# Kernel tuning notes

Hardware: AMD Instinct MI355X
Metric: run time of the kernel (lower is better)

Reference implementation:

```python
import jax, jax.numpy as jnp
import numpy as np

T_HID, A_HID, V_HID = 256, 128, 128
LEN = T_HID + A_HID + V_HID            # 512
TIME_WINDOW = 2
EXT_DIM = TIME_WINDOW * LEN + 1        # 1025
RANK, OUT_DIM = 128, 16
STRIDE = 2
B, T = 256, 128
T_IN, A_IN, V_IN = 768, 74, 35


def _mk_lstm(key, d_in, h):
    k1, k2, k3 = jax.random.split(key, 3)
    s = 1.0 / np.sqrt(h)
    W_ih = jax.random.uniform(k1, (4 * h, d_in), jnp.float32, -s, s)
    W_hh = jax.random.uniform(k2, (4 * h, h), jnp.float32, -s, s)
    b = jax.random.uniform(k3, (4 * h,), jnp.float32, -s, s)
    return W_ih, W_hh, b


def setup_inputs() -> dict:
    key = jax.random.key(0)
    ks = jax.random.split(key, 10)
    inp = {
        "text_x": jax.random.normal(ks[0], (B, T, T_IN), jnp.float32),
        "audio_x": jax.random.normal(ks[1], (B, T, A_IN), jnp.float32),
        "video_x": jax.random.normal(ks[2], (B, T, V_IN), jnp.float32),
    }
    inp["W_ih_t"], inp["W_hh_t"], inp["b_t"] = _mk_lstm(ks[3], T_IN, T_HID)
    inp["W_ih_a"], inp["W_hh_a"], inp["b_a"] = _mk_lstm(ks[4], A_IN, A_HID)
    inp["W_ih_v"], inp["W_hh_v"], inp["b_v"] = _mk_lstm(ks[5], V_IN, V_HID)
    ro = RANK * OUT_DIM
    inp["W1"] = jax.random.normal(ks[6], (ro, LEN), jnp.float32) / np.sqrt(LEN)
    inp["b1"] = jnp.zeros((ro,), jnp.float32)
    inp["W2"] = jax.random.normal(ks[7], (ro, EXT_DIM), jnp.float32) / np.sqrt(EXT_DIM)
    inp["b2"] = jnp.zeros((ro,), jnp.float32)
    inp["fusion_w"] = jax.random.normal(ks[8], (1, RANK), jnp.float32) * np.sqrt(2.0 / (1 + RANK))
    return inp


def _lstm(x, W_ih, W_hh, b, h):
    # x: [B,T,D] -> all hidden states [B,T,H]; PyTorch gate order i,f,g,o
    xp = jnp.einsum('btd,gd->btg', x, W_ih) + b  # [B,T,4H]
    h0 = jnp.zeros((x.shape[0], h), x.dtype)

    def step(carry, xt):
        hp, cp = carry
        g = xt + hp @ W_hh.T
        i, f, gg, o = jnp.split(g, 4, axis=-1)
        c = jax.nn.sigmoid(f) * cp + jax.nn.sigmoid(i) * jnp.tanh(gg)
        hn = jax.nn.sigmoid(o) * jnp.tanh(c)
        return (hn, c), hn

    _, hs = jax.lax.scan(step, (h0, h0), jnp.swapaxes(xp, 0, 1))
    return jnp.swapaxes(hs, 0, 1)


def reference(text_x, audio_x, video_x,
              W_ih_t, W_hh_t, b_t, W_ih_a, W_hh_a, b_a, W_ih_v, W_hh_v, b_v,
              W1, b1, W2, b2, fusion_w):
    audio_h = _lstm(audio_x, W_ih_a, W_hh_a, b_a, A_HID)
    video_h = _lstm(video_x, W_ih_v, W_hh_v, b_v, V_HID)
    text_h = _lstm(text_x, W_ih_t, W_hh_t, b_t, T_HID)
    z = jnp.concatenate((audio_h, video_h, text_h), axis=2)  # [B,T,LEN]

    # time_extend with circular wraparound: [B,T,1+W*LEN]
    tidx = (jnp.arange(T)[:, None] + jnp.arange(TIME_WINDOW)[None, :]) % T  # [T,W]
    z_ext = z[:, tidx, :].reshape(z.shape[0], T, TIME_WINDOW * LEN)
    ones = jnp.ones((z.shape[0], T, 1), z.dtype)
    z_ext = jnp.concatenate((ones, z_ext), axis=2)  # [B,T,EXT_DIM]

    idx = jnp.arange(0, T, STRIDE)  # strided fusion steps
    zi = z[:, idx, :]               # [B,K,LEN]
    ze = z_ext[:, idx, :]           # [B,K,EXT_DIM]
    f1 = jnp.einsum('bkd,rd->bkr', zi, W1) + b1
    f2 = jnp.einsum('bkd,rd->bkr', ze, W2) + b2
    z_fusion = jnp.mean(f1 * f2, axis=1)  # sum_i (.)/len(idx)  -> [B, RANK*OUT]
    z_fusion = z_fusion.reshape(-1, RANK, OUT_DIM)
    output = jnp.einsum('r,bro->bo', fusion_w[0], z_fusion)
    return output
```

## Files before the change

### kernel.cpp

```cpp
#include <hip/hip_runtime.h>
#include <hip/hip_bf16.h>
#include <math.h>


typedef __attribute__((ext_vector_type(8))) short short8;
typedef __attribute__((ext_vector_type(4))) float f32x4;

__device__ __forceinline__ float sigm(float x) { return 1.0f / (1.0f + __expf(-x)); }
__device__ __forceinline__ float tanh_(float x) {
    float ax = fabsf(x);
    float e  = __expf(-2.0f * ax);
    float t  = (1.0f - e) / (1.0f + e);
    return copysignf(t, x);
}
__device__ __forceinline__ ushort f2bf(float x) {
    __hip_bfloat16 h = __float2bfloat16(x);
    return *reinterpret_cast<ushort*>(&h);
}
__device__ __forceinline__ float bf2f(ushort u) { return __uint_as_float(((unsigned)u) << 16); }

__device__ __forceinline__ void gl_lds16(const void* g, void* l) {
    __builtin_amdgcn_global_load_lds(
        (const __attribute__((address_space(1))) unsigned int*)g,
        (__attribute__((address_space(3))) unsigned int*)l, 16, 0, 0);
}

#define BARRIER_LIGHT() \
    do { asm volatile("s_waitcnt lgkmcnt(0)" ::: "memory"); \
         __builtin_amdgcn_s_barrier(); \
         asm volatile("" ::: "memory"); } while (0)

__global__ __launch_bounds__(256) void gemm_mfma(
    const float* __restrict__ A, const float* __restrict__ W,
    const float* __restrict__ bias, ushort* __restrict__ C,
    int M, int N, int K)
{
    constexpr int STR = 40;
    __shared__ ushort As[128 * STR];
    __shared__ ushort Ws[128 * STR];

    const int tid  = threadIdx.x;
    const int lane = tid & 63;
    const int wave = tid >> 6;
    const int bm   = blockIdx.y * 128;
    const int bn   = blockIdx.x * 128;
    const int m0   = (wave >> 1) * 64;
    const int n0   = (wave & 1) * 64;
    const int row  = tid >> 1;
    const int kseg = (tid & 1) * 16;
    const int fr   = lane & 15;
    const int fk   = (lane >> 4) * 8;

    f32x4 acc[4][4];
#pragma unroll
    for (int i = 0; i < 4; ++i)
#pragma unroll
        for (int j = 0; j < 4; ++j) acc[i][j] = (f32x4)(0.f);

    const bool kmul4 = (K & 3) == 0;

    for (int k0 = 0; k0 < K; k0 += 32) {
        {
            const float* ap = A + (size_t)(bm + row) * K + k0 + kseg;
            if (kmul4 && (k0 + kseg + 16) <= K) {
                float4 v0 = *(const float4*)ap;
                float4 v1 = *(const float4*)(ap + 4);
                float4 v2 = *(const float4*)(ap + 8);
                float4 v3 = *(const float4*)(ap + 12);
                short8 o0, o1;
                o0[0]=f2bf(v0.x); o0[1]=f2bf(v0.y); o0[2]=f2bf(v0.z); o0[3]=f2bf(v0.w);
                o0[4]=f2bf(v1.x); o0[5]=f2bf(v1.y); o0[6]=f2bf(v1.z); o0[7]=f2bf(v1.w);
                o1[0]=f2bf(v2.x); o1[1]=f2bf(v2.y); o1[2]=f2bf(v2.z); o1[3]=f2bf(v2.w);
                o1[4]=f2bf(v3.x); o1[5]=f2bf(v3.y); o1[6]=f2bf(v3.z); o1[7]=f2bf(v3.w);
                *(short8*)&As[row * STR + kseg]     = o0;
                *(short8*)&As[row * STR + kseg + 8] = o1;
            } else {
#pragma unroll
                for (int j = 0; j < 16; ++j) {
                    int kk = k0 + kseg + j;
                    As[row * STR + kseg + j] = (kk < K) ? f2bf(ap[j]) : (ushort)0;
                }
            }
        }
        {
            const float* wp = W + (size_t)(bn + row) * K + k0 + kseg;
            if (kmul4 && (k0 + kseg + 16) <= K) {
                float4 v0 = *(const float4*)wp;
                float4 v1 = *(const float4*)(wp + 4);
                float4 v2 = *(const float4*)(wp + 8);
                float4 v3 = *(const float4*)(wp + 12);
                short8 o0, o1;
                o0[0]=f2bf(v0.x); o0[1]=f2bf(v0.y); o0[2]=f2bf(v0.z); o0[3]=f2bf(v0.w);
                o0[4]=f2bf(v1.x); o0[5]=f2bf(v1.y); o0[6]=f2bf(v1.z); o0[7]=f2bf(v1.w);
                o1[0]=f2bf(v2.x); o1[1]=f2bf(v2.y); o1[2]=f2bf(v2.z); o1[3]=f2bf(v2.w);
                o1[4]=f2bf(v3.x); o1[5]=f2bf(v3.y); o1[6]=f2bf(v3.z); o1[7]=f2bf(v3.w);
                *(short8*)&Ws[row * STR + kseg]     = o0;
                *(short8*)&Ws[row * STR + kseg + 8] = o1;
            } else {
#pragma unroll
                for (int j = 0; j < 16; ++j) {
                    int kk = k0 + kseg + j;
                    Ws[row * STR + kseg + j] = (kk < K) ? f2bf(wp[j]) : (ushort)0;
                }
            }
        }
        __syncthreads();

        short8 af[4], wf[4];
#pragma unroll
        for (int mi = 0; mi < 4; ++mi)
            af[mi] = *(const short8*)&As[(m0 + mi * 16 + fr) * STR + fk];
#pragma unroll
        for (int ni = 0; ni < 4; ++ni)
            wf[ni] = *(const short8*)&Ws[(n0 + ni * 16 + fr) * STR + fk];
#pragma unroll
        for (int mi = 0; mi < 4; ++mi)
#pragma unroll
            for (int ni = 0; ni < 4; ++ni)
                acc[mi][ni] = __builtin_amdgcn_mfma_f32_16x16x32_bf16(
                    af[mi], wf[ni], acc[mi][ni], 0, 0, 0);
        __syncthreads();
    }

#pragma unroll
    for (int ni = 0; ni < 4; ++ni) {
        const int col = bn + n0 + ni * 16 + fr;
        const float bb = bias[col];
#pragma unroll
        for (int mi = 0; mi < 4; ++mi)
#pragma unroll
            for (int q = 0; q < 4; ++q) {
                int r  = bm + m0 + mi * 16 + (lane >> 4) * 4 + q;
                int b  = r >> 7, t = r & 127;
                size_t idx;
                if (N == 1024) {
                    int g = col >> 8, w = (col >> 5) & 7, s = (col >> 4) & 1, pl = col & 15;
                    idx = ((((size_t)(b >> 4) * 128 + t) * 8 + w) * 8 + (g * 2 + s)) * 256
                        + (size_t)(b & 15) * 16 + pl;
                } else {
                    int g = col >> 7, w = (col >> 4) & 7, pl = col & 15;
                    idx = ((((size_t)(b >> 4) * 128 + t) * 8 + w) * 4 + g) * 256
                        + (size_t)(b & 15) * 16 + pl;
                }
                C[idx] = f2bf(acc[mi][ni][q] + bb);
            }
    }
}

__global__ void wfrag_pack(const float* __restrict__ Wt, const float* __restrict__ Wa,
                           const float* __restrict__ Wv, ushort* __restrict__ WFt,
                           ushort* __restrict__ WFa, ushort* __restrict__ WFv)
{
    int idx = blockIdx.x * 256 + threadIdx.x;
    if (idx < 262144) {
        int e = idx;
        int jj = e & 7, n = (e >> 3) & 15, k8 = (e >> 7) & 3;
        int ti = e >> 9;
        int gs = ti & 7, w = (ti >> 3) & 7, kt = ti >> 6;
        int g = gs >> 1, s = gs & 1;
        WFt[e] = f2bf(Wt[(size_t)(g * 256 + w * 32 + s * 16 + n) * 256 + kt * 32 + k8 * 8 + jj]);
    } else if (idx < 327680) {
        int e = idx - 262144;
        int jj = e & 7, k8 = (e >> 3) & 3, n = (e >> 5) & 15;
        int g = (e >> 9) & 3, w = (e >> 11) & 7, kt = (e >> 14) & 3;
        WFa[e] = f2bf(Wa[(size_t)(g * 128 + w * 16 + n) * 128 + kt * 32 + k8 * 8 + jj]);
    } else if (idx < 393216) {
        int e = idx - 327680;
        int jj = e & 7, k8 = (e >> 3) & 3, n = (e >> 5) & 15;
        int g = (e >> 9) & 3, w = (e >> 11) & 7, kt = (e >> 14) & 3;
        WFv[e] = f2bf(Wv[(size_t)(g * 128 + w * 16 + n) * 128 + kt * 32 + k8 * 8 + jj]);
    }
}

__global__ void wf_pack(const float* __restrict__ W1, const float* __restrict__ W2,
                        ushort* __restrict__ W1b, ushort* __restrict__ W2ab,
                        ushort* __restrict__ W2bb)
{
    int idx = blockIdx.x * 256 + threadIdx.x;
    if (idx >= 1048576) return;
    int r = idx >> 9, c = idx & 511;
    W1b[idx]  = f2bf(W1[idx]);
    W2ab[idx] = f2bf(W2[(size_t)r * 1025 + 1 + c]);
    W2bb[idx] = f2bf(W2[(size_t)r * 1025 + 513 + c]);
}

#define STAGE_W(KT)                                                                \
    do {                                                                           \
        const char* gs_ = (const char*)WFt + (size_t)(((KT) * 8 + w) * 8) * 1024   \
                          + lane * 16;                                             \
        char* ld_ = wbuf + ((KT) & 1) * 8192;                                      \
        _Pragma("unroll") for (int e_ = 0; e_ < 8; ++e_)                           \
            gl_lds16(gs_ + e_ * 1024, ld_ + e_ * 1024);                            \
    } while (0)

#define TEXT_STEP(T, XC, XN, RP)                                                   \
    do {                                                                           \
        f32x4 acc[8];                                                              \
        _Pragma("unroll") for (int e = 0; e < 8; ++e) acc[e] = (f32x4)(0.f);       \
        _Pragma("unroll") for (int kt = 0; kt < 8; ++kt) {                         \
            if (kt < 2) { asm volatile("s_waitcnt vmcnt(16)" ::: "memory"); }      \
            else        { asm volatile("s_waitcnt vmcnt(8)" ::: "memory"); }       \
            __builtin_amdgcn_sched_barrier(0);                                     \
            short8 wt[8];                                                          \
            _Pragma("unroll") for (int e = 0; e < 8; ++e)                          \
                wt[e] = *(const short8*)(wbuf + (kt & 1) * 8192 + e * 1024 + lane * 16); \
            short8 hfk;                                                           \
            { int byt = (RP) * 8192 + np * 512 + kt * 64 + k8 * 16;                \
              hfk = *(const short8*)(hbase + (byt ^ ((np & 7) << 4))); }           \
            asm volatile("s_waitcnt lgkmcnt(0)" ::: "memory");                     \
            __builtin_amdgcn_sched_barrier(0);                                     \
            STAGE_W((kt + 2) & 7);                                                 \
            __builtin_amdgcn_sched_barrier(0);                                     \
            _Pragma("unroll") for (int e = 0; e < 8; ++e)                          \
                acc[e] = __builtin_amdgcn_mfma_f32_16x16x32_bf16(wt[e], hfk, acc[e], 0, 0, 0); \
        }                                                                          \
        _Pragma("unroll") for (int e = 0; e < 8; ++e) {                            \
            acc[e][0] += bf2f((ushort)((XC)[e].x & 0xffffu));                      \
            acc[e][1] += bf2f((ushort)((XC)[e].x >> 16));                          \
            acc[e][2] += bf2f((ushort)((XC)[e].y & 0xffffu));                      \
            acc[e][3] += bf2f((ushort)((XC)[e].y >> 16));                          \
        }                                                                          \
        uint2 hw[2];                                                               \
        _Pragma("unroll") for (int s = 0; s < 2; ++s) {                            \
            ushort hq[4];                                                          \
            _Pragma("unroll") for (int q = 0; q < 4; ++q) {                        \
                float iv = acc[0 + s][q], fv = acc[2 + s][q];                      \
                float gv = acc[4 + s][q], ov = acc[6 + s][q];                      \
                float cc = sigm(fv) * c_st[s][q] + sigm(iv) * tanh_(gv);           \
                c_st[s][q] = cc;                                                   \
                hq[q] = f2bf(sigm(ov) * tanh_(cc));                                \
            }                                                                      \
            hw[s].x = (uint)hq[0] | ((uint)hq[1] << 16);                           \
            hw[s].y = (uint)hq[2] | ((uint)hq[3] << 16);                           \
        }                                                                          \
        __builtin_amdgcn_sched_barrier(0);                                         \
        _Pragma("unroll") for (int s = 0; s < 2; ++s) {                            \
            int byt = ((RP) ^ 1) * 8192 + np * 512 + w * 64 + s * 32 + k8 * 8;     \
            *(uint2*)(hbase + (byt ^ ((np & 7) << 4))) = hw[s];                    \
            *(uint2*)(zb + zrow + (size_t)(T) * 512 + s * 16) = hw[s];             \
        }                                                                          \
        { const ushort* xrn = xbase + (size_t)(((T) + 1) & 127) * 16384;           \
          _Pragma("unroll") for (int e = 0; e < 8; ++e)                            \
              (XN)[e] = *(const uint2*)(xrn + e * 256); }                          \
        __builtin_amdgcn_sched_barrier(0);                                         \
        BARRIER_LIGHT();                                                           \
    } while (0)

#define AV_STEP(T, XC, XN, RP)                                                     \
    do {                                                                           \
        short8 hf[4];                                                              \
        _Pragma("unroll") for (int kt = 0; kt < 4; ++kt) {                         \
            int byt = (RP) * 4096 + np * 256 + kt * 64 + k8 * 16;                  \
            hf[kt] = *(const short8*)(hbase + (byt ^ ((np & 7) << 4)));            \
        }                                                                          \
        f32x4 acc[4];                                                              \
        _Pragma("unroll") for (int g = 0; g < 4; ++g) acc[g] = (f32x4)(0.f);       \
        _Pragma("unroll") for (int kt = 0; kt < 4; ++kt)                           \
            _Pragma("unroll") for (int g = 0; g < 4; ++g)                          \
                acc[g] = __builtin_amdgcn_mfma_f32_16x16x32_bf16(wres[kt][g], hf[kt], acc[g], 0, 0, 0); \
        { const ushort* xrn = xbase + (size_t)(((T) + 1) & 127) * 8192;            \
          _Pragma("unroll") for (int g = 0; g < 4; ++g)                            \
              (XN)[g] = *(const uint2*)(xrn + g * 256); }                          \
        _Pragma("unroll") for (int g = 0; g < 4; ++g) {                            \
            acc[g][0] += bf2f((ushort)((XC)[g].x & 0xffffu));                      \
            acc[g][1] += bf2f((ushort)((XC)[g].x >> 16));                          \
            acc[g][2] += bf2f((ushort)((XC)[g].y & 0xffffu));                      \
            acc[g][3] += bf2f((ushort)((XC)[g].y >> 16));                          \
        }                                                                          \
        ushort hq[4];                                                              \
        _Pragma("unroll") for (int q = 0; q < 4; ++q) {                            \
            float cc = sigm(acc[1][q]) * c_st0[q] + sigm(acc[0][q]) * tanh_(acc[2][q]); \
            c_st0[q] = cc;                                                         \
            hq[q] = f2bf(sigm(acc[3][q]) * tanh_(cc));                             \
        }                                                                          \
        uint2 hw;                                                                  \
        hw.x = (uint)hq[0] | ((uint)hq[1] << 16);                                  \
        hw.y = (uint)hq[2] | ((uint)hq[3] << 16);                                  \
        {                                                                          \
            int byt = ((RP) ^ 1) * 4096 + np * 256 + w * 32 + k8 * 8;              \
            *(uint2*)(hbase + (byt ^ ((np & 7) << 4))) = hw;                       \
            *(uint2*)(zb + zrow + (size_t)(T) * 512) = hw;                         \
        }                                                                          \
        BARRIER_LIGHT();                                                           \
    } while (0)

__global__ __launch_bounds__(512) void lstm_mfma5(
    const ushort* __restrict__ xpt, const ushort* __restrict__ xpa,
    const ushort* __restrict__ xpv, const ushort* __restrict__ WFt,
    const ushort* __restrict__ WFa, const ushort* __restrict__ WFv,
    ushort* __restrict__ zb)
{
    __shared__ __align__(16) char smem[147456];
    const int tid  = threadIdx.x;
    const int lane = tid & 63;
    const int w    = tid >> 6;
    const int np   = lane & 15;
    const int k8   = lane >> 4;
    const int bid  = blockIdx.x;
    char* hbase = smem;
    char* wbuf  = smem + 16384 + w * 16384;

    if (bid < 16) {
        const int bt = bid;
        const ushort* xbase = xpt + (size_t)bt * 2097152 + w * 2048 + np * 16 + k8 * 4;
        const size_t  zrow  = ((size_t)(bt * 16 + np) * 128) * 512 + 256 + w * 32 + k8 * 4;

        STAGE_W(0);
        STAGE_W(1);
        uint2 xvA[8], xvB[8];
#pragma unroll
        for (int e = 0; e < 8; ++e) xvA[e] = *(const uint2*)(xbase + e * 256);

        for (int i = tid; i < 4096; i += 512) ((uint*)hbase)[i] = 0u;
        float c_st[2][4];
#pragma unroll
        for (int s = 0; s < 2; ++s)
#pragma unroll
            for (int q = 0; q < 4; ++q) c_st[s][q] = 0.f;
        __syncthreads();

#pragma unroll 1
        for (int t = 0; t < 128; t += 2) {
            TEXT_STEP(t,     xvA, xvB, 0);
            TEXT_STEP(t + 1, xvB, xvA, 1);
        }
    } else {
        const bool isA = bid < 32;
        const int bt = bid - (isA ? 16 : 32);
        const ushort* xp = isA ? xpa : xpv;
        const ushort* WF = isA ? WFa : WFv;
        const int zoff = isA ? 0 : 128;

        short8 wres[4][4];
#pragma unroll
        for (int kt = 0; kt < 4; ++kt)
#pragma unroll
            for (int g = 0; g < 4; ++g)
                wres[kt][g] = *(const short8*)(WF + (size_t)((kt * 8 + w) * 4 + g) * 512 + np * 32 + k8 * 8);
        for (int i = tid; i < 2048; i += 512) ((uint*)hbase)[i] = 0u;
        float c_st0[4];
#pragma unroll
        for (int q = 0; q < 4; ++q) c_st0[q] = 0.f;
        __syncthreads();

        const ushort* xbase = xp + (size_t)bt * 1048576 + w * 1024 + np * 16 + k8 * 4;
        const size_t  zrow  = ((size_t)(bt * 16 + np) * 128) * 512 + zoff + w * 16 + k8 * 4;

        uint2 xvA[4], xvB[4];
#pragma unroll
        for (int g = 0; g < 4; ++g) xvA[g] = *(const uint2*)(xbase + g * 256);

#pragma unroll 1
        for (int t = 0; t < 128; t += 2) {
            AV_STEP(t,     xvA, xvB, 0);
            AV_STEP(t + 1, xvB, xvA, 1);
        }
    }
}

__global__ __launch_bounds__(256) void fuse_mfma(
    const ushort* __restrict__ zb, const ushort* __restrict__ W1b,
    const ushort* __restrict__ W2ab, const ushort* __restrict__ W2bb,
    const float* __restrict__ b1, const float* __restrict__ b2,
    const float* __restrict__ W2, float* __restrict__ zf)
{
    constexpr int STR = 40;
    __shared__ ushort As[64 * STR];
    __shared__ ushort W1s[256 * STR];
    __shared__ ushort W2s[256 * STR];

    const int tid  = threadIdx.x;
    const int lane = tid & 63;
    const int wave = tid >> 6;
    const int b    = blockIdx.y;
    const int r0   = blockIdx.x * 256;
    const int n0w  = wave * 64;

    const int a_row  = tid >> 2;
    const int a_c8   = (tid & 3) * 8;
    const int fr_row = lane & 15;
    const int fr_k   = (lane >> 4) * 8;

    f32x4 acc1[4][4], acc2[4][4];
#pragma unroll
    for (int i = 0; i < 4; ++i)
#pragma unroll
        for (int j = 0; j < 4; ++j) {
            acc1[i][j] = (f32x4)(0.f);
            acc2[i][j] = (f32x4)(0.f);
        }

    for (int pass = 0; pass < 2; ++pass) {
        const ushort* wsrc = pass ? W2bb : W2ab;
        for (int c0 = 0; c0 < 512; c0 += 32) {
            {
                const int4 v = *(const int4*)(zb +
                    (((size_t)b * 128 + 2 * a_row + pass) * 512 + c0 + a_c8));
                *(int4*)&As[a_row * STR + a_c8] = v;
            }
            if (pass == 0) {
                const ushort* w1p = W1b + (size_t)(r0 + tid) * 512 + c0;
#pragma unroll
                for (int j = 0; j < 4; ++j)
                    *(int4*)&W1s[tid * STR + j * 8] = *(const int4*)(w1p + j * 8);
            }
            {
                const ushort* w2p = wsrc + (size_t)(r0 + tid) * 512 + c0;
#pragma unroll
                for (int j = 0; j < 4; ++j)
                    *(int4*)&W2s[tid * STR + j * 8] = *(const int4*)(w2p + j * 8);
            }
            __syncthreads();

            short8 af[4], w2f[4];
#pragma unroll
            for (int mi = 0; mi < 4; ++mi)
                af[mi] = *(const short8*)&As[(mi * 16 + fr_row) * STR + fr_k];
#pragma unroll
            for (int ni = 0; ni < 4; ++ni)
                w2f[ni] = *(const short8*)&W2s[(n0w + ni * 16 + fr_row) * STR + fr_k];

            if (pass == 0) {
                short8 w1f[4];
#pragma unroll
                for (int ni = 0; ni < 4; ++ni)
                    w1f[ni] = *(const short8*)&W1s[(n0w + ni * 16 + fr_row) * STR + fr_k];
#pragma unroll
                for (int mi = 0; mi < 4; ++mi)
#pragma unroll
                    for (int ni = 0; ni < 4; ++ni) {
                        acc1[mi][ni] = __builtin_amdgcn_mfma_f32_16x16x32_bf16(
                            af[mi], w1f[ni], acc1[mi][ni], 0, 0, 0);
                        acc2[mi][ni] = __builtin_amdgcn_mfma_f32_16x16x32_bf16(
                            af[mi], w2f[ni], acc2[mi][ni], 0, 0, 0);
                    }
            } else {
#pragma unroll
                for (int mi = 0; mi < 4; ++mi)
#pragma unroll
                    for (int ni = 0; ni < 4; ++ni)
                        acc2[mi][ni] = __builtin_amdgcn_mfma_f32_16x16x32_bf16(
                            af[mi], w2f[ni], acc2[mi][ni], 0, 0, 0);
            }
            __syncthreads();
        }
    }

#pragma unroll
    for (int ni = 0; ni < 4; ++ni) {
        const int r = r0 + n0w + ni * 16 + fr_row;
        const float bb1 = b1[r];
        const float bb2 = b2[r] + W2[(size_t)r * 1025];
        float s = 0.f;
#pragma unroll
        for (int mi = 0; mi < 4; ++mi)
#pragma unroll
            for (int q = 0; q < 4; ++q)
                s += (acc1[mi][ni][q] + bb1) * (acc2[mi][ni][q] + bb2);
        s += __shfl_xor(s, 16);
        s += __shfl_xor(s, 32);
        if ((lane >> 4) == 0)
            zf[(size_t)b * 2048 + r] = s * (1.0f / 64.0f);
    }
}

__global__ void final_out(const float* __restrict__ zf, const float* __restrict__ fw,
                          float* __restrict__ out)
{
    int idx = blockIdx.x * 256 + threadIdx.x;
    int b = idx >> 4, o = idx & 15;
    float s = 0.f;
#pragma unroll
    for (int r = 0; r < 128; ++r)
        s = fmaf(fw[r], zf[(size_t)b * 2048 + r * 16 + o], s);
    out[idx] = s;
}

extern "C" void kernel_launch(void* const* d_in, const int* in_sizes, int n_in,
                              void* d_out, int out_size, void* d_ws, size_t ws_size,
                              hipStream_t stream)
{
    const float* text_x  = (const float*)d_in[0];
    const float* audio_x = (const float*)d_in[1];
    const float* video_x = (const float*)d_in[2];
    const float* W_ih_t  = (const float*)d_in[3];
    const float* W_hh_t  = (const float*)d_in[4];
    const float* b_t     = (const float*)d_in[5];
    const float* W_ih_a  = (const float*)d_in[6];
    const float* W_hh_a  = (const float*)d_in[7];
    const float* b_a     = (const float*)d_in[8];
    const float* W_ih_v  = (const float*)d_in[9];
    const float* W_hh_v  = (const float*)d_in[10];
    const float* b_v     = (const float*)d_in[11];
    const float* W1      = (const float*)d_in[12];
    const float* b1      = (const float*)d_in[13];
    const float* W2      = (const float*)d_in[14];
    const float* b2      = (const float*)d_in[15];
    const float* fw      = (const float*)d_in[16];
    float* out = (float*)d_out;

    char* base = (char*)d_ws;
    ushort* xpt  = (ushort*)(base);
    ushort* xpa  = (ushort*)(base + 67108864);
    ushort* xpv  = (ushort*)(base + 100663296);
    ushort* zbuf = (ushort*)(base + 134217728);
    ushort* WFt  = (ushort*)(base + 167772160);
    ushort* WFa  = (ushort*)(base + 168296448);
    ushort* WFv  = (ushort*)(base + 168427520);
    ushort* W1b  = (ushort*)(base + 168558592);
    ushort* W2ab = (ushort*)(base + 170655744);
    ushort* W2bb = (ushort*)(base + 172752896);
    float*  zf   = (float*)(base + 174850048);

    gemm_mfma<<<dim3(8, 256), 256, 0, stream>>>(text_x,  W_ih_t, b_t, xpt, 32768, 1024, 768);
    gemm_mfma<<<dim3(4, 256), 256, 0, stream>>>(audio_x, W_ih_a, b_a, xpa, 32768, 512, 74);
    gemm_mfma<<<dim3(4, 256), 256, 0, stream>>>(video_x, W_ih_v, b_v, xpv, 32768, 512, 35);
    wfrag_pack<<<1536, 256, 0, stream>>>(W_hh_t, W_hh_a, W_hh_v, WFt, WFa, WFv);
    wf_pack<<<4096, 256, 0, stream>>>(W1, W2, W1b, W2ab, W2bb);
    lstm_mfma5<<<48, 512, 0, stream>>>(xpt, xpa, xpv, WFt, WFa, WFv, zbuf);
    fuse_mfma<<<dim3(8, 256), 256, 0, stream>>>(zbuf, W1b, W2ab, W2bb, b1, b2, W2, zf);
    final_out<<<16, 256, 0, stream>>>(zf, fw, out);
}
```

Measured before the change: 1.668 ms.

## Split text LSTM hidden units across four blocks with global flag synchronization

The text LSTM is restructured so each group of 64 batch rows is handled by four cooperating blocks, each owning a quarter of the hidden units. Each block keeps its W_hh slice resident in LDS instead of streaming it every step. The blocks exchange h through global memory and synchronize per timestep with atomic flags, and the xp and W layouts are repacked to match. This removes the per-step weight streaming but adds inter-block spin-wait latency and global round-trips on every one of the 128 steps, and it relies on all blocks being co-resident.

```diff
diff --git a/kernel.cpp b/kernel.cpp
--- a/kernel.cpp
+++ b/kernel.cpp
@@ -134,12 +134,15 @@
                 int b  = r >> 7, t = r & 127;
                 size_t idx;
                 if (N == 1024) {
-                    int g = col >> 8, w = (col >> 5) & 7, s = (col >> 4) & 1, pl = col & 15;
-                    idx = ((((size_t)(b >> 4) * 128 + t) * 8 + w) * 8 + (g * 2 + s)) * 256
-                        + (size_t)(b & 15) * 16 + pl;
+                    int g = col >> 8, pos = col & 255;
+                    int psx = pos >> 6, p = pos & 63;
+                    int wq = p >> 3, grtx = (p >> 2) & 1, k8x = p & 3;
+                    int bgx = b >> 6, bl = b & 63, btx = bl >> 4, npx = bl & 15;
+                    idx = (size_t)(bgx * 128 + t) * 65536 + (size_t)psx * 16384
+                        + wq * 2048 + grtx * 1024 + btx * 256 + npx * 16 + k8x * 4 + g;
                 } else {
-                    int g = col >> 7, w = (col >> 4) & 7, pl = col & 15;
-                    idx = ((((size_t)(b >> 4) * 128 + t) * 8 + w) * 4 + g) * 256
+                    int g = col >> 7, wq = (col >> 4) & 7, pl = col & 15;
+                    idx = ((((size_t)(b >> 4) * 128 + t) * 8 + wq) * 4 + g) * 256
                         + (size_t)(b & 15) * 16 + pl;
                 }
                 C[idx] = f2bf(acc[mi][ni][q] + bb);
@@ -154,11 +157,12 @@
     int idx = blockIdx.x * 256 + threadIdx.x;
     if (idx < 262144) {
         int e = idx;
-        int jj = e & 7, n = (e >> 3) & 15, k8 = (e >> 7) & 3;
-        int ti = e >> 9;
-        int gs = ti & 7, w = (ti >> 3) & 7, kt = ti >> 6;
-        int g = gs >> 1, s = gs & 1;
-        WFt[e] = f2bf(Wt[(size_t)(g * 256 + w * 32 + s * 16 + n) * 256 + kt * 32 + k8 * 8 + jj]);
+        int ps = e >> 16, rem = e & 65535, r = rem >> 8, kk = rem & 255;
+        int g = r & 3, p = r >> 2;
+        int n = g * 256 + ps * 64 + p;
+        int pu = ((kk >> 3) + 4 * r) & 31;
+        WFt[(size_t)ps * 65536 + r * 256 + pu * 8 + (kk & 7)] =
+            f2bf(Wt[(size_t)n * 256 + kk]);
     } else if (idx < 327680) {
         int e = idx - 262144;
         int jj = e & 7, k8 = (e >> 3) & 3, n = (e >> 5) & 15;
@@ -184,67 +188,10 @@
     W2bb[idx] = f2bf(W2[(size_t)r * 1025 + 513 + c]);
 }
 
-#define STAGE_W(KT)                                                                \
-    do {                                                                           \
-        const char* gs_ = (const char*)WFt + (size_t)(((KT) * 8 + w) * 8) * 1024   \
-                          + lane * 16;                                             \
-        char* ld_ = wbuf + ((KT) & 1) * 8192;                                      \
-        _Pragma("unroll") for (int e_ = 0; e_ < 8; ++e_)                           \
-            gl_lds16(gs_ + e_ * 1024, ld_ + e_ * 1024);                            \
-    } while (0)
-
-#define TEXT_STEP(T, XC, XN, RP)                                                   \
-    do {                                                                           \
-        f32x4 acc[8];                                                              \
-        _Pragma("unroll") for (int e = 0; e < 8; ++e) acc[e] = (f32x4)(0.f);       \
-        _Pragma("unroll") for (int kt = 0; kt < 8; ++kt) {                         \
-            if (kt < 2) { asm volatile("s_waitcnt vmcnt(16)" ::: "memory"); }      \
-            else        { asm volatile("s_waitcnt vmcnt(8)" ::: "memory"); }       \
-            __builtin_amdgcn_sched_barrier(0);                                     \
-            short8 wt[8];                                                          \
-            _Pragma("unroll") for (int e = 0; e < 8; ++e)                          \
-                wt[e] = *(const short8*)(wbuf + (kt & 1) * 8192 + e * 1024 + lane * 16); \
-            short8 hfk;                                                           \
-            { int byt = (RP) * 8192 + np * 512 + kt * 64 + k8 * 16;                \
-              hfk = *(const short8*)(hbase + (byt ^ ((np & 7) << 4))); }           \
-            asm volatile("s_waitcnt lgkmcnt(0)" ::: "memory");                     \
-            __builtin_amdgcn_sched_barrier(0);                                     \
-            STAGE_W((kt + 2) & 7);                                                 \
-            __builtin_amdgcn_sched_barrier(0);                                     \
-            _Pragma("unroll") for (int e = 0; e < 8; ++e)                          \
-                acc[e] = __builtin_amdgcn_mfma_f32_16x16x32_bf16(wt[e], hfk, acc[e], 0, 0, 0); \
-        }                                                                          \
-        _Pragma("unroll") for (int e = 0; e < 8; ++e) {                            \
-            acc[e][0] += bf2f((ushort)((XC)[e].x & 0xffffu));                      \
-            acc[e][1] += bf2f((ushort)((XC)[e].x >> 16));                          \
-            acc[e][2] += bf2f((ushort)((XC)[e].y & 0xffffu));                      \
-            acc[e][3] += bf2f((ushort)((XC)[e].y >> 16));                          \
-        }                                                                          \
-        uint2 hw[2];                                                               \
-        _Pragma("unroll") for (int s = 0; s < 2; ++s) {                            \
-            ushort hq[4];                                                          \
-            _Pragma("unroll") for (int q = 0; q < 4; ++q) {                        \
-                float iv = acc[0 + s][q], fv = acc[2 + s][q];                      \
-                float gv = acc[4 + s][q], ov = acc[6 + s][q];                      \
-                float cc = sigm(fv) * c_st[s][q] + sigm(iv) * tanh_(gv);           \
-                c_st[s][q] = cc;                                                   \
-                hq[q] = f2bf(sigm(ov) * tanh_(cc));                                \
-            }                                                                      \
-            hw[s].x = (uint)hq[0] | ((uint)hq[1] << 16);                           \
-            hw[s].y = (uint)hq[2] | ((uint)hq[3] << 16);                           \
-        }                                                                          \
-        __builtin_amdgcn_sched_barrier(0);                                         \
-        _Pragma("unroll") for (int s = 0; s < 2; ++s) {                            \
-            int byt = ((RP) ^ 1) * 8192 + np * 512 + w * 64 + s * 32 + k8 * 8;     \
-            *(uint2*)(hbase + (byt ^ ((np & 7) << 4))) = hw[s];                    \
-            *(uint2*)(zb + zrow + (size_t)(T) * 512 + s * 16) = hw[s];             \
-        }                                                                          \
-        { const ushort* xrn = xbase + (size_t)(((T) + 1) & 127) * 16384;           \
-          _Pragma("unroll") for (int e = 0; e < 8; ++e)                            \
-              (XN)[e] = *(const uint2*)(xrn + e * 256); }                          \
-        __builtin_amdgcn_sched_barrier(0);                                         \
-        BARRIER_LIGHT();                                                           \
-    } while (0)
+__global__ void zero_flags(int* flags) {
+    int i = blockIdx.x * 256 + threadIdx.x;
+    if (i < 512) flags[i] = 0;
+}
 
 #define AV_STEP(T, XC, XN, RP)                                                     \
     do {                                                                           \
@@ -284,47 +231,137 @@
         BARRIER_LIGHT();                                                           \
     } while (0)
 
-__global__ __launch_bounds__(512) void lstm_mfma5(
+__global__ __launch_bounds__(512) void lstm_mfma6(
     const ushort* __restrict__ xpt, const ushort* __restrict__ xpa,
     const ushort* __restrict__ xpv, const ushort* __restrict__ WFt,
     const ushort* __restrict__ WFa, const ushort* __restrict__ WFv,
-    ushort* __restrict__ zb)
-{
-    __shared__ __align__(16) char smem[147456];
+    ushort* __restrict__ zb, int* __restrict__ flags)
+{
+    __shared__ __align__(16) char smem[131072];
     const int tid  = threadIdx.x;
     const int lane = tid & 63;
     const int w    = tid >> 6;
     const int np   = lane & 15;
     const int k8   = lane >> 4;
     const int bid  = blockIdx.x;
-    char* hbase = smem;
-    char* wbuf  = smem + 16384 + w * 16384;
 
     if (bid < 16) {
-        const int bt = bid;
-        const ushort* xbase = xpt + (size_t)bt * 2097152 + w * 2048 + np * 16 + k8 * 4;
-        const size_t  zrow  = ((size_t)(bt * 16 + np) * 128) * 512 + 256 + w * 32 + k8 * 4;
-
-        STAGE_W(0);
-        STAGE_W(1);
-        uint2 xvA[8], xvB[8];
-#pragma unroll
-        for (int e = 0; e < 8; ++e) xvA[e] = *(const uint2*)(xbase + e * 256);
-
-        for (int i = tid; i < 4096; i += 512) ((uint*)hbase)[i] = 0u;
+        const int bg = bid >> 2, ps = bid & 3;
+        {
+            const char* wg = (const char*)WFt + (size_t)ps * 131072 + w * 16384 + lane * 16;
+            char* wl = smem + w * 16384;
+#pragma unroll
+            for (int i = 0; i < 16; ++i) gl_lds16(wg + i * 1024, wl + i * 1024);
+        }
+        asm volatile("s_waitcnt vmcnt(0)" ::: "memory");
+        __syncthreads();
+
         float c_st[2][4];
 #pragma unroll
-        for (int s = 0; s < 2; ++s)
-#pragma unroll
-            for (int q = 0; q < 4; ++q) c_st[s][q] = 0.f;
-        __syncthreads();
+        for (int g2 = 0; g2 < 2; ++g2)
+#pragma unroll
+            for (int q = 0; q < 4; ++q) c_st[g2][q] = 0.f;
+
+        const ushort* xthr = xpt + (size_t)bg * 128 * 65536 + (size_t)ps * 16384
+                             + w * 2048 + np * 16 + k8 * 4;
+        const ushort* zrd0 = zb + ((size_t)(bg * 64 + np) * 128) * 512 + 256 + k8 * 8;
+        ushort*       zwr0 = zb + ((size_t)(bg * 64 + np) * 128) * 512 + 256
+                             + ps * 64 + w * 8 + k8;
+        const int w32 = w * 32;
+        int* const flg = flags + bg * 128;
 
 #pragma unroll 1
-        for (int t = 0; t < 128; t += 2) {
-            TEXT_STEP(t,     xvA, xvB, 0);
-            TEXT_STEP(t + 1, xvB, xvA, 1);
+        for (int t = 0; t < 128; ++t) {
+            if (t > 0) {
+                if (tid == 0) {
+                    while (atomicAdd(&flg[t - 1], 0) < 4) __builtin_amdgcn_s_sleep(2);
+                }
+                __syncthreads();
+                __threadfence();
+            }
+            uint2 xv[8];
+            {
+                const ushort* xr = xthr + (size_t)t * 65536;
+#pragma unroll
+                for (int grt = 0; grt < 2; ++grt)
+#pragma unroll
+                    for (int bt = 0; bt < 4; ++bt)
+                        xv[grt * 4 + bt] = *(const uint2*)(xr + grt * 1024 + bt * 256);
+            }
+            f32x4 acc[2][4];
+#pragma unroll
+            for (int grt = 0; grt < 2; ++grt)
+#pragma unroll
+                for (int bt = 0; bt < 4; ++bt) acc[grt][bt] = (f32x4)(0.f);
+
+            if (t > 0) {
+                const ushort* zr = zrd0 + (size_t)(t - 1) * 512;
+                short8 bA[4], bB[4];
+#pragma unroll
+                for (int bt = 0; bt < 4; ++bt)
+                    bA[bt] = *(const short8*)(zr + (size_t)bt * 1048576);
+#pragma unroll
+                for (int kt = 0; kt < 8; ++kt) {
+                    if (kt < 7) {
+                        if ((kt & 1) == 0) {
+#pragma unroll
+                            for (int bt = 0; bt < 4; ++bt)
+                                bB[bt] = *(const short8*)(zr + (size_t)bt * 1048576 + (kt + 1) * 32);
+                        } else {
+#pragma unroll
+                            for (int bt = 0; bt < 4; ++bt)
+                                bA[bt] = *(const short8*)(zr + (size_t)bt * 1048576 + (kt + 1) * 32);
+                        }
+                    }
+                    const int row0 = w32 + np;
+                    const int row1 = w32 + 16 + np;
+                    short8 wa0 = *(const short8*)(smem + row0 * 512 +
+                                    (((kt * 4 + k8 + row0 * 4) & 31) << 4));
+                    short8 wa1 = *(const short8*)(smem + row1 * 512 +
+                                    (((kt * 4 + k8 + row1 * 4) & 31) << 4));
+                    asm volatile("s_waitcnt lgkmcnt(0)" ::: "memory");
+                    __builtin_amdgcn_sched_barrier(0);
+                    if (kt < 7) { asm volatile("s_waitcnt vmcnt(4)" ::: "memory"); }
+                    else        { asm volatile("s_waitcnt vmcnt(0)" ::: "memory"); }
+                    __builtin_amdgcn_sched_barrier(0);
+                    if ((kt & 1) == 0) {
+#pragma unroll
+                        for (int bt = 0; bt < 4; ++bt) {
+                            acc[0][bt] = __builtin_amdgcn_mfma_f32_16x16x32_bf16(wa0, bA[bt], acc[0][bt], 0, 0, 0);
+                            acc[1][bt] = __builtin_amdgcn_mfma_f32_16x16x32_bf16(wa1, bA[bt], acc[1][bt], 0, 0, 0);
+                        }
+                    } else {
+#pragma unroll
+                        for (int bt = 0; bt < 4; ++bt) {
+                            acc[0][bt] = __builtin_amdgcn_mfma_f32_16x16x32_bf16(wa0, bB[bt], acc[0][bt], 0, 0, 0);
+                            acc[1][bt] = __builtin_amdgcn_mfma_f32_16x16x32_bf16(wa1, bB[bt], acc[1][bt], 0, 0, 0);
+                        }
+                    }
+                }
+            } else {
+                asm volatile("s_waitcnt vmcnt(0)" ::: "memory");
+            }
+
+            ushort* zw = zwr0 + (size_t)t * 512;
+#pragma unroll
+            for (int grt = 0; grt < 2; ++grt)
+#pragma unroll
+                for (int bt = 0; bt < 4; ++bt) {
+                    const uint2 xq = xv[grt * 4 + bt];
+                    float iv = acc[grt][bt][0] + bf2f((ushort)(xq.x & 0xffffu));
+                    float fv = acc[grt][bt][1] + bf2f((ushort)(xq.x >> 16));
+                    float gv = acc[grt][bt][2] + bf2f((ushort)(xq.y & 0xffffu));
+                    float ov = acc[grt][bt][3] + bf2f((ushort)(xq.y >> 16));
+                    float cc = sigm(fv) * c_st[grt][bt] + sigm(iv) * tanh_(gv);
+                    c_st[grt][bt] = cc;
+                    zw[(size_t)bt * 1048576 + grt * 4] = f2bf(sigm(ov) * tanh_(cc));
+                }
+            __threadfence();
+            __syncthreads();
+            if (tid == 0) atomicAdd(&flg[t], 1);
         }
     } else {
+        char* hbase = smem;
         const bool isA = bid < 32;
         const int bt = bid - (isA ? 16 : 32);
         const ushort* xp = isA ? xpa : xpv;
@@ -511,13 +548,15 @@
     ushort* W2ab = (ushort*)(base + 170655744);
     ushort* W2bb = (ushort*)(base + 172752896);
     float*  zf   = (float*)(base + 174850048);
+    int*    flgs = (int*)(base + 176947200);
 
     gemm_mfma<<<dim3(8, 256), 256, 0, stream>>>(text_x,  W_ih_t, b_t, xpt, 32768, 1024, 768);
     gemm_mfma<<<dim3(4, 256), 256, 0, stream>>>(audio_x, W_ih_a, b_a, xpa, 32768, 512, 74);
     gemm_mfma<<<dim3(4, 256), 256, 0, stream>>>(video_x, W_ih_v, b_v, xpv, 32768, 512, 35);
     wfrag_pack<<<1536, 256, 0, stream>>>(W_hh_t, W_hh_a, W_hh_v, WFt, WFa, WFv);
     wf_pack<<<4096, 256, 0, stream>>>(W1, W2, W1b, W2ab, W2bb);
-    lstm_mfma5<<<48, 512, 0, stream>>>(xpt, xpa, xpv, WFt, WFa, WFv, zbuf);
+    zero_flags<<<2, 256, 0, stream>>>(flgs);
+    lstm_mfma6<<<48, 512, 0, stream>>>(xpt, xpa, xpv, WFt, WFa, WFv, zbuf, flgs);
     fuse_mfma<<<dim3(8, 256), 256, 0, stream>>>(zbuf, W1b, W2ab, W2bb, b1, b2, W2, zf);
     final_out<<<16, 256, 0, stream>>>(zf, fw, out);
 }
```

Measured after the change: 2.617 ms. +56.9%, slower.
